# Optimization experiments

Hardware: AMD Instinct MI355X
Metric: run time of the kernel (lower is better)

The kernel has to match this reference:

```python
import jax, jax.numpy as jnp
import numpy as np
import math

B, L, D_MODEL, D_K, H = 2, 1024, 1024, 1024, 16
HD = D_K // H  # 64, even
EPS = 1e-5


def setup_inputs() -> dict:
    key = jax.random.key(0)
    ks = jax.random.split(key, 16)
    s = 0.02
    inp = {
        'word_embed': jax.random.normal(ks[0], (B, L, D_MODEL), jnp.float32),
        'speaker_embed': jax.random.normal(ks[1], (B, L, D_MODEL), jnp.float32),
        'mask': jnp.broadcast_to(jnp.tril(jnp.ones((L, L), jnp.int32)), (B, L, L)),
        'qw_w': jax.random.normal(ks[2], (D_K, D_MODEL), jnp.float32) * s,
        'qw_b': jnp.zeros((D_K,), jnp.float32),
        'kw_w': jax.random.normal(ks[3], (D_K, D_MODEL), jnp.float32) * s,
        'kw_b': jnp.zeros((D_K,), jnp.float32),
        'qs_w': jax.random.normal(ks[4], (D_K, D_MODEL), jnp.float32) * s,
        'qs_b': jnp.zeros((D_K,), jnp.float32),
        'ks_w': jax.random.normal(ks[5], (D_K, D_MODEL), jnp.float32) * s,
        'ks_b': jnp.zeros((D_K,), jnp.float32),
        'v_w': jax.random.normal(ks[6], (D_K, D_MODEL), jnp.float32) * s,
        'v_b': jnp.zeros((D_K,), jnp.float32),
        'out_w': jax.random.normal(ks[7], (D_MODEL, D_K), jnp.float32) * s,
        'out_b': jnp.zeros((D_MODEL,), jnp.float32),
        'gamma': jnp.ones((HD,), jnp.float32),
        'beta': jnp.zeros((HD,), jnp.float32),
    }
    return inp


def _rotary_tables(seq_len, dim, dtype):
    pos = jnp.arange(seq_len, dtype=dtype)[:, None]  # [L,1]
    div = jnp.exp(jnp.arange(0, dim, 2, dtype=dtype) * (-math.log(10000.0) / dim))
    return jnp.sin(pos * div), jnp.cos(pos * div)  # each [L, dim//2]


def _rotary(x, sin, cos):
    # x: [B,H,L,HD]; NOTE: original concatenates halves (non-interleaved output)
    x1, x2 = x[..., 0::2], x[..., 1::2]
    return jnp.concatenate([x1 * cos - x2 * sin, x1 * sin + x2 * cos], axis=-1)


def _layernorm(x, gamma, beta):
    mu = jnp.mean(x, axis=-1, keepdims=True)
    var = jnp.mean(jnp.square(x - mu), axis=-1, keepdims=True)
    return (x - mu) * jax.lax.rsqrt(var + EPS) * gamma + beta


def _split(x):
    b, l, _ = x.shape
    return x.reshape(b, l, H, HD).transpose(0, 2, 1, 3)  # [B,H,L,HD]


def reference(word_embed, speaker_embed, mask, qw_w, qw_b, kw_w, kw_b,
              qs_w, qs_b, ks_w, ks_b, v_w, v_b, out_w, out_b, gamma, beta):
    proj = lambda x, w, b: jnp.einsum('bld,kd->blk', x, w) + b
    qw = _split(proj(word_embed, qw_w, qw_b))
    kw = _split(proj(word_embed, kw_w, kw_b))
    qs = _split(proj(speaker_embed, qs_w, qs_b))
    ks = _split(proj(speaker_embed, ks_w, ks_b))
    v = _split(proj(word_embed, v_w, v_b))

    sin, cos = _rotary_tables(word_embed.shape[1], HD, word_embed.dtype)
    ln = lambda x: _layernorm(_rotary(x, sin, cos), gamma, beta)
    qw, kw, qs, ks = ln(qw), ln(kw), ln(qs), ln(ks)

    scores = (jnp.einsum('bhqd,bhkd->bhqk', qw, kw)
              + jnp.einsum('bhqd,bhkd->bhqk', qs, ks)) / math.sqrt(2 * HD)
    scores = jnp.where(mask[:, None] == 0, -jnp.inf, scores)
    attn = jax.nn.softmax(scores, axis=-1)  # dropout is eval-mode no-op
    out = jnp.einsum('bhqk,bhkd->bhqd', attn, v)
    out = out.transpose(0, 2, 1, 3).reshape(out.shape[0], out.shape[2], D_K)
    out = jnp.einsum('blk,dk->bld', out, out_w) + out_b
    return (out, attn)
```

## Files before the change

### kernel.cpp

```cpp
#include <hip/hip_runtime.h>
#include <cstdint>
#include <cstddef>

typedef __bf16 bf16x8 __attribute__((ext_vector_type(8)));
typedef float  f32x4  __attribute__((ext_vector_type(4)));
typedef unsigned short ushort8_t __attribute__((ext_vector_type(8)));

__device__ __forceinline__ unsigned short f2bf(float f){
  unsigned u = __builtin_bit_cast(unsigned, f);
  u += 0x7fffu + ((u >> 16) & 1u);
  return (unsigned short)(u >> 16);
}
__device__ __forceinline__ float bf2f(unsigned short s){
  return __builtin_bit_cast(float, ((unsigned)s) << 16);
}

#define MFMA16(a,b,c) __builtin_amdgcn_mfma_f32_16x16x32_bf16((a),(b),(c),0,0,0)

__device__ __forceinline__ void gload16(const void* g, void* lds){
  __builtin_amdgcn_global_load_lds(
      (const __attribute__((address_space(1))) void*)g,
      (__attribute__((address_space(3))) void*)lds, 16, 0, 0);
}

#define E_XW    ((size_t)0)
#define E_XS    (E_XW    + (size_t)2048*1024)
#define E_WWORD (E_XS    + (size_t)2048*1024)
#define E_WSPK  (E_WWORD + (size_t)3072*1024)
#define E_WOUT  (E_WSPK  + (size_t)2048*1024)
#define E_PWORD (E_WOUT  + (size_t)1024*1024)
#define E_PSPK  (E_PWORD + (size_t)2048*3072)
#define E_VT    (E_PSPK  + (size_t)2048*2048)
#define E_CTX   (E_VT    + (size_t)2048*1024)
#define E_END   (E_CTX   + (size_t)2048*1024)

__global__ __launch_bounds__(256) void convert_all(
    const float* __restrict__ word, const float* __restrict__ spk,
    const float* __restrict__ qww,  const float* __restrict__ kww,
    const float* __restrict__ vw,   const float* __restrict__ qsw,
    const float* __restrict__ ksw,  const float* __restrict__ outw,
    const float* __restrict__ qwb,  const float* __restrict__ kwb,
    const float* __restrict__ vb,   const float* __restrict__ qsb,
    const float* __restrict__ ksb,
    unsigned short* __restrict__ wsb, float* __restrict__ FB)
{
  int idx = blockIdx.x*256 + threadIdx.x;
  if (idx < 32768){
    int pos = idx >> 5, i = idx & 31;
    float inv = expf((float)(2*i) * -0.14391157f);
    float ang = (float)pos * inv;
    float sv, cv; sincosf(ang, &sv, &cv);
    FB[5120 + idx]         = sv;
    FB[5120 + 32768 + idx] = cv;
  } else if (idx < 33792){
    int i = idx - 32768;
    FB[i] = qwb[i]; FB[1024+i] = kwb[i]; FB[2048+i] = vb[i];
    FB[3072+i] = qsb[i]; FB[3072+1024+i] = ksb[i];
  }

  const size_t total = 2621440;
  for (size_t c = (size_t)blockIdx.x*256 + threadIdx.x; c < total;
       c += (size_t)gridDim.x*256){
    const float* src; size_t dst; size_t i;
    if (c < 524288)       { src = word; dst = E_XW; i = c; }
    else if (c < 1048576) { src = spk;  dst = E_XS; i = c - 524288; }
    else {
      size_t t = c - 1048576; int seg = (int)(t >> 18); i = t & 262143;
      switch (seg){
        case 0:  src = qww; dst = E_WWORD;                      break;
        case 1:  src = kww; dst = E_WWORD + (size_t)1048576;    break;
        case 2:  src = vw;  dst = E_WWORD + (size_t)2097152;    break;
        case 3:  src = qsw; dst = E_WSPK;                       break;
        case 4:  src = ksw; dst = E_WSPK  + (size_t)1048576;    break;
        default: src = outw; dst = E_WOUT;                      break;
      }
    }
    float4 v = ((const float4*)src)[i];
    ushort4 o; o.x = f2bf(v.x); o.y = f2bf(v.y); o.z = f2bf(v.z); o.w = f2bf(v.w);
    ((ushort4*)(wsb + dst))[i] = o;
  }
}

template<int NF>
__device__ __forceinline__ void gemm_body(
    const unsigned short* __restrict__ A, const unsigned short* __restrict__ Bw,
    const float* __restrict__ bias, void* __restrict__ Cv,
    int N, int bid, int out_bf16,
    unsigned short* As, unsigned short* Bs)
{
  const int K = 1024;
  const int BN = NF*32;
  const int nbn = N / BN;
  const int bm = bid / nbn, bn = bid % nbn;
  const int tid = threadIdx.x;
  const int l = tid & 63, w = tid >> 6;
  const int wm = w >> 1, wn = w & 1;
  const int li = l & 15, lg = l >> 4;

  f32x4 acc[4][NF];
  #pragma unroll
  for (int a = 0; a < 4; a++)
    #pragma unroll
    for (int b = 0; b < NF; b++) acc[a][b] = (f32x4){0.f,0.f,0.f,0.f};

  const int colS = (l & 3) * 8;
  const size_t aBase = (size_t)(bm*128) * K;
  const size_t bBase = (size_t)(bn*BN) * K;

  for (int kt = 0; kt < K; kt += 32){
    #pragma unroll
    for (int j = 0; j < 2; j++){
      int row = (w*2 + j)*16 + (l >> 2);
      gload16(A + aBase + (size_t)row*K + kt + colS, &As[(size_t)(w*2+j)*512]);
    }
    if (NF == 4){
      #pragma unroll
      for (int j = 0; j < 2; j++){
        int row = (w*2 + j)*16 + (l >> 2);
        gload16(Bw + bBase + (size_t)row*K + kt + colS, &Bs[(size_t)(w*2+j)*512]);
      }
    } else {
      int row = w*16 + (l >> 2);
      gload16(Bw + bBase + (size_t)row*K + kt + colS, &Bs[(size_t)w*512]);
    }
    asm volatile("s_waitcnt vmcnt(0)" ::: "memory");
    __syncthreads();

    bf16x8 af[4], bfr[NF];
    const int ko = lg * 8;
    #pragma unroll
    for (int fm = 0; fm < 4; fm++)
      af[fm] = *(const bf16x8*)&As[(wm*64 + fm*16 + li)*32 + ko];
    #pragma unroll
    for (int fn = 0; fn < NF; fn++)
      bfr[fn] = *(const bf16x8*)&Bs[(wn*(NF*16) + fn*16 + li)*32 + ko];
    #pragma unroll
    for (int fm = 0; fm < 4; fm++)
      #pragma unroll
      for (int fn = 0; fn < NF; fn++)
        acc[fm][fn] = MFMA16(af[fm], bfr[fn], acc[fm][fn]);
    __syncthreads();
  }

  #pragma unroll
  for (int fm = 0; fm < 4; fm++){
    int m0 = bm*128 + wm*64 + fm*16 + lg*4;
    #pragma unroll
    for (int fn = 0; fn < NF; fn++){
      int n = bn*BN + wn*(NF*16) + fn*16 + li;
      float bv = bias[n];
      #pragma unroll
      for (int r = 0; r < 4; r++){
        float v = acc[fm][fn][r] + bv;
        if (out_bf16) ((unsigned short*)Cv)[(size_t)(m0+r)*N + n] = f2bf(v);
        else          ((float*)Cv)[(size_t)(m0+r)*N + n] = v;
      }
    }
  }
}

__global__ __launch_bounds__(256) void gemm_qkv(
    const unsigned short* __restrict__ XW, const unsigned short* __restrict__ WWORD,
    const unsigned short* __restrict__ XS, const unsigned short* __restrict__ WSPK,
    const float* __restrict__ FB,
    unsigned short* __restrict__ PWORD, unsigned short* __restrict__ PSPK)
{
  __shared__ unsigned short As[128*32];
  __shared__ unsigned short Bs[128*32];
  int raw = blockIdx.x;
  int bid = (raw & 7)*80 + (raw >> 3);
  if (bid < 384)
    gemm_body<4>(XW, WWORD, FB,        PWORD, 3072, bid,       1, As, Bs);
  else
    gemm_body<4>(XS, WSPK,  FB + 3072, PSPK,  2048, bid - 384, 1, As, Bs);
}

__global__ __launch_bounds__(256) void gemm_out(
    const unsigned short* __restrict__ CTX, const unsigned short* __restrict__ WOUT,
    const float* __restrict__ outb, float* __restrict__ outp)
{
  __shared__ unsigned short As[128*32];
  __shared__ unsigned short Bs[64*32];
  int raw = blockIdx.x;
  int bid = (raw & 7)*32 + (raw >> 3);
  gemm_body<2>(CTX, WOUT, outb, outp, 1024, bid, 0, As, Bs);
}

__global__ __launch_bounds__(256) void postproc(
    unsigned short* __restrict__ Pw, unsigned short* __restrict__ Ps,
    const float* __restrict__ gamma, const float* __restrict__ beta,
    const float* __restrict__ TS, const float* __restrict__ TC,
    unsigned short* __restrict__ VT)
{
  __shared__ float lds[2320];
  int bx = blockIdx.x;
  int t = threadIdx.x;
  if (bx < 4096){
    int sec = bx & 3, rp = bx >> 2;
    int half = t >> 7, c = t & 127;
    int row = rp*2 + half;
    int seg = c >> 3, j = c & 7;
    unsigned short* p;
    if      (sec == 0) p = Pw + (size_t)row*3072 +        seg*64;
    else if (sec == 1) p = Pw + (size_t)row*3072 + 1024 + seg*64;
    else if (sec == 2) p = Ps + (size_t)row*2048 +        seg*64;
    else               p = Ps + (size_t)row*2048 + 1024 + seg*64;
    int pos = row & 1023;
    int sl  = half*16 + seg;

    ushort8_t xv = *(const ushort8_t*)(p + j*8);
    float4 sv = *(const float4*)&TS[pos*32 + j*4];
    float4 cv = *(const float4*)&TC[pos*32 + j*4];
    float ss[4] = {sv.x, sv.y, sv.z, sv.w};
    float cc[4] = {cv.x, cv.y, cv.z, cv.w};
    float y1[4], y2[4];
    #pragma unroll
    for (int k = 0; k < 4; k++){
      float x0 = bf2f(xv[2*k]), x1 = bf2f(xv[2*k+1]);
      y1[k] = x0*cc[k] - x1*ss[k];
      y2[k] = x0*ss[k] + x1*cc[k];
    }
    *(float4*)&lds[sl*68 + j*4]      = (float4){y1[0], y1[1], y1[2], y1[3]};
    *(float4*)&lds[sl*68 + 32 + j*4] = (float4){y2[0], y2[1], y2[2], y2[3]};
    __syncthreads();

    float4 a0 = *(const float4*)&lds[sl*68 + j*8];
    float4 a1 = *(const float4*)&lds[sl*68 + j*8 + 4];
    float v[8] = {a0.x, a0.y, a0.z, a0.w, a1.x, a1.y, a1.z, a1.w};
    float s = 0.f;
    #pragma unroll
    for (int k = 0; k < 8; k++) s += v[k];
    #pragma unroll
    for (int o = 1; o < 8; o <<= 1) s += __shfl_xor(s, o);
    float mu = s * (1.f/64.f);
    float sq = 0.f;
    #pragma unroll
    for (int k = 0; k < 8; k++){ float d = v[k] - mu; sq += d*d; }
    #pragma unroll
    for (int o = 1; o < 8; o <<= 1) sq += __shfl_xor(sq, o);
    float rs = rsqrtf(sq * (1.f/64.f) + 1e-5f);
    float4 g0 = *(const float4*)&gamma[j*8], g1 = *(const float4*)&gamma[j*8+4];
    float4 b0 = *(const float4*)&beta[j*8],  b1 = *(const float4*)&beta[j*8+4];
    float gg[8] = {g0.x,g0.y,g0.z,g0.w,g1.x,g1.y,g1.z,g1.w};
    float bb[8] = {b0.x,b0.y,b0.z,b0.w,b1.x,b1.y,b1.z,b1.w};
    ushort8_t o8;
    #pragma unroll
    for (int k = 0; k < 8; k++) o8[k] = f2bf((v[k]-mu)*rs*gg[k] + bb[k]);
    *(ushort8_t*)(p + j*8) = o8;
  } else {
    unsigned short* tp = (unsigned short*)lds;
    int bid2 = bx - 4096;
    int bh = bid2 >> 4, lt = bid2 & 15;
    int b = bh >> 4, h = bh & 15;
    #pragma unroll
    for (int i = 0; i < 2; i++){
      int cc2 = t + i*256;
      int row = cc2 >> 3, co = (cc2 & 7)*8;
      const unsigned short* src = Pw + (size_t)(b*1024 + lt*64 + row)*3072 + 2048 + h*64 + co;
      *(uint4*)&tp[row*72 + co] = *(const uint4*)src;
    }
    __syncthreads();
    int d = t >> 2, jb = (t & 3)*16;
    unsigned short o[16];
    #pragma unroll
    for (int j = 0; j < 16; j++) o[j] = tp[(jb + j)*72 + d];
    unsigned short* dst = VT + ((size_t)bh*64 + d)*1024 + lt*64 + jb;
    *(uint4*)dst       = *(uint4*)&o[0];
    *(uint4*)(dst + 8) = *(uint4*)&o[8];
  }
}

__global__ __launch_bounds__(256) void attn_fused(
    const unsigned short* __restrict__ Pw, const unsigned short* __restrict__ Ps,
    const unsigned short* __restrict__ VTg,
    float* __restrict__ attn, unsigned short* __restrict__ Ctx)
{
  __shared__ unsigned short SL[32256];

  int raw = blockIdx.x;
  int bx  = (raw & 7)*64 + (raw >> 3);
  int b = bx >> 8, rem = bx & 255, h = rem >> 4;
  int qt = 15 - (rem & 15);
  int tid = threadIdx.x;
  int w = tid >> 6, l = tid & 63;
  int lg = l >> 4, li = l & 15;
  int q0 = qt*64 + w*16;
  int bh = b*16 + h;

  int sr = tid >> 3, sc = tid & 7;
  const unsigned short* gKW = Pw + (size_t)(b*1024)*3072 + 1024 + h*64;
  const unsigned short* gKS = Ps + (size_t)(b*1024)*2048 + 1024 + h*64;
  const unsigned short* gVT = VTg + (size_t)bh*64*1024;
  unsigned short* pt = SL + 27648 + w*1152;

  bf16x8 aqw[2], aqs[2];
  {
    int q = q0 + li;
    const unsigned short* pqw = Pw + (size_t)(b*1024 + q)*3072 + h*64 + lg*8;
    const unsigned short* pqs = Ps + (size_t)(b*1024 + q)*2048 + h*64 + lg*8;
    aqw[0] = *(const bf16x8*)pqw;  aqw[1] = *(const bf16x8*)(pqw + 32);
    aqs[0] = *(const bf16x8*)pqs;  aqs[1] = *(const bf16x8*)(pqs + 32);
  }
  const float rscale = 0.08838834764831845f;

  uint4 ka0, ka1, kb0, kb1, va0, va1;

  float ps4[4] = {0.f, 0.f, 0.f, 0.f};
  ka0 = *(const uint4*)(gKW + (size_t)sr*3072 + sc*8);
  ka1 = *(const uint4*)(gKW + (size_t)(sr+32)*3072 + sc*8);
  kb0 = *(const uint4*)(gKS + (size_t)sr*2048 + sc*8);
  kb1 = *(const uint4*)(gKS + (size_t)(sr+32)*2048 + sc*8);
  *(uint4*)(SL + sr*72 + sc*8) = ka0;
  *(uint4*)(SL + (sr+32)*72 + sc*8) = ka1;
  *(uint4*)(SL + 9216 + sr*72 + sc*8) = kb0;
  *(uint4*)(SL + 9216 + (sr+32)*72 + sc*8) = kb1;

  for (int kt = 0; kt <= qt; ++kt){
    int buf = kt & 1;
    if (kt < qt){
      ka0 = *(const uint4*)(gKW + (size_t)((kt+1)*64 + sr)*3072 + sc*8);
      ka1 = *(const uint4*)(gKW + (size_t)((kt+1)*64 + sr+32)*3072 + sc*8);
      kb0 = *(const uint4*)(gKS + (size_t)((kt+1)*64 + sr)*2048 + sc*8);
      kb1 = *(const uint4*)(gKS + (size_t)((kt+1)*64 + sr+32)*2048 + sc*8);
    }
    __syncthreads();
    {
      const unsigned short* KWt = SL + buf*4608;
      const unsigned short* KSt = SL + 9216 + buf*4608;
      f32x4 s[4];
      #pragma unroll
      for (int fn = 0; fn < 4; fn++){
        s[fn] = (f32x4){0.f,0.f,0.f,0.f};
        int rr = (fn*16 + li)*72;
        bf16x8 k0 = *(const bf16x8*)(KWt + rr + lg*8);
        bf16x8 k1 = *(const bf16x8*)(KWt + rr + 32 + lg*8);
        bf16x8 k2 = *(const bf16x8*)(KSt + rr + lg*8);
        bf16x8 k3 = *(const bf16x8*)(KSt + rr + 32 + lg*8);
        s[fn] = MFMA16(aqw[0], k0, s[fn]);
        s[fn] = MFMA16(aqw[1], k1, s[fn]);
        s[fn] = MFMA16(aqs[0], k2, s[fn]);
        s[fn] = MFMA16(aqs[1], k3, s[fn]);
      }
      #pragma unroll
      for (int r = 0; r < 4; r++){
        int q = q0 + lg*4 + r;
        #pragma unroll
        for (int fn = 0; fn < 4; fn++){
          int k = kt*64 + fn*16 + li;
          float e = __expf(s[fn][r] * rscale);
          ps4[r] += (k <= q) ? e : 0.f;
        }
      }
    }
    if (kt < qt){
      int nb = buf ^ 1;
      *(uint4*)(SL + nb*4608 + sr*72 + sc*8) = ka0;
      *(uint4*)(SL + nb*4608 + (sr+32)*72 + sc*8) = ka1;
      *(uint4*)(SL + 9216 + nb*4608 + sr*72 + sc*8) = kb0;
      *(uint4*)(SL + 9216 + nb*4608 + (sr+32)*72 + sc*8) = kb1;
    }
  }
  #pragma unroll
  for (int r = 0; r < 4; r++){
    #pragma unroll
    for (int o = 1; o < 16; o <<= 1) ps4[r] += __shfl_xor(ps4[r], o);
  }
  float rinv[4];
  #pragma unroll
  for (int r = 0; r < 4; r++) rinv[r] = 1.f / ps4[r];

  __syncthreads();
  ka0 = *(const uint4*)(gKW + (size_t)sr*3072 + sc*8);
  ka1 = *(const uint4*)(gKW + (size_t)(sr+32)*3072 + sc*8);
  kb0 = *(const uint4*)(gKS + (size_t)sr*2048 + sc*8);
  kb1 = *(const uint4*)(gKS + (size_t)(sr+32)*2048 + sc*8);
  va0 = *(const uint4*)(gVT + (size_t)sr*1024 + sc*8);
  va1 = *(const uint4*)(gVT + (size_t)(sr+32)*1024 + sc*8);
  *(uint4*)(SL + sr*72 + sc*8) = ka0;
  *(uint4*)(SL + (sr+32)*72 + sc*8) = ka1;
  *(uint4*)(SL + 9216 + sr*72 + sc*8) = kb0;
  *(uint4*)(SL + 9216 + (sr+32)*72 + sc*8) = kb1;
  *(uint4*)(SL + 18432 + sr*72 + sc*8) = va0;
  *(uint4*)(SL + 18432 + (sr+32)*72 + sc*8) = va1;

  f32x4 c[4];
  #pragma unroll
  for (int fn = 0; fn < 4; fn++) c[fn] = (f32x4){0.f,0.f,0.f,0.f};

  for (int kt = 0; kt <= qt; ++kt){
    int buf = kt & 1;
    if (kt < qt){
      ka0 = *(const uint4*)(gKW + (size_t)((kt+1)*64 + sr)*3072 + sc*8);
      ka1 = *(const uint4*)(gKW + (size_t)((kt+1)*64 + sr+32)*3072 + sc*8);
      kb0 = *(const uint4*)(gKS + (size_t)((kt+1)*64 + sr)*2048 + sc*8);
      kb1 = *(const uint4*)(gKS + (size_t)((kt+1)*64 + sr+32)*2048 + sc*8);
      va0 = *(const uint4*)(gVT + (size_t)sr*1024 + (kt+1)*64 + sc*8);
      va1 = *(const uint4*)(gVT + (size_t)(sr+32)*1024 + (kt+1)*64 + sc*8);
    }
    __syncthreads();
    float* abase = attn + ((size_t)bh*1024 + q0 + li)*1024 + kt*64;
    {
      const unsigned short* KWt = SL + buf*4608;
      const unsigned short* KSt = SL + 9216 + buf*4608;
      const unsigned short* VTt = SL + 18432 + buf*4608;
      f32x4 s[4];
      #pragma unroll
      for (int fn = 0; fn < 4; fn++){
        s[fn] = (f32x4){0.f,0.f,0.f,0.f};
        int rr = (fn*16 + li)*72;
        bf16x8 k0 = *(const bf16x8*)(KWt + rr + lg*8);
        bf16x8 k1 = *(const bf16x8*)(KWt + rr + 32 + lg*8);
        bf16x8 k2 = *(const bf16x8*)(KSt + rr + lg*8);
        bf16x8 k3 = *(const bf16x8*)(KSt + rr + 32 + lg*8);
        s[fn] = MFMA16(aqw[0], k0, s[fn]);
        s[fn] = MFMA16(aqw[1], k1, s[fn]);
        s[fn] = MFMA16(aqs[0], k2, s[fn]);
        s[fn] = MFMA16(aqs[1], k3, s[fn]);
      }
      #pragma unroll
      for (int fn = 0; fn < 4; fn++){
        #pragma unroll
        for (int r = 0; r < 4; r++){
          int k = kt*64 + fn*16 + li;
          int q = q0 + lg*4 + r;
          float pp = (k <= q) ? __expf(s[fn][r] * rscale) * rinv[r] : 0.f;
          pt[(lg*4 + r)*72 + fn*16 + li] = f2bf(pp);
        }
      }
      asm volatile("s_waitcnt lgkmcnt(0)" ::: "memory");
      __builtin_amdgcn_sched_barrier(0);
      bf16x8 af0 = *(const bf16x8*)(pt + li*72 + lg*8);
      bf16x8 af1 = *(const bf16x8*)(pt + li*72 + 32 + lg*8);
      ushort8_t u0 = __builtin_bit_cast(ushort8_t, af0);
      ushort8_t u1 = __builtin_bit_cast(ushort8_t, af1);
      *(float4*)(abase + lg*8)          = (float4){bf2f(u0[0]),bf2f(u0[1]),bf2f(u0[2]),bf2f(u0[3])};
      *(float4*)(abase + lg*8 + 4)      = (float4){bf2f(u0[4]),bf2f(u0[5]),bf2f(u0[6]),bf2f(u0[7])};
      *(float4*)(abase + 32 + lg*8)     = (float4){bf2f(u1[0]),bf2f(u1[1]),bf2f(u1[2]),bf2f(u1[3])};
      *(float4*)(abase + 32 + lg*8 + 4) = (float4){bf2f(u1[4]),bf2f(u1[5]),bf2f(u1[6]),bf2f(u1[7])};
      #pragma unroll
      for (int fn = 0; fn < 4; fn++){
        int rr = (fn*16 + li)*72;
        bf16x8 v0 = *(const bf16x8*)(VTt + rr + lg*8);
        bf16x8 v1 = *(const bf16x8*)(VTt + rr + 32 + lg*8);
        c[fn] = MFMA16(af0, v0, c[fn]);
        c[fn] = MFMA16(af1, v1, c[fn]);
      }
    }
    if (kt < qt){
      int nb = buf ^ 1;
      *(uint4*)(SL + nb*4608 + sr*72 + sc*8) = ka0;
      *(uint4*)(SL + nb*4608 + (sr+32)*72 + sc*8) = ka1;
      *(uint4*)(SL + 9216 + nb*4608 + sr*72 + sc*8) = kb0;
      *(uint4*)(SL + 9216 + nb*4608 + (sr+32)*72 + sc*8) = kb1;
      *(uint4*)(SL + 18432 + nb*4608 + sr*72 + sc*8) = va0;
      *(uint4*)(SL + 18432 + nb*4608 + (sr+32)*72 + sc*8) = va1;
    }
  }

  for (int kt = qt + 1; kt < 16; ++kt){
    float* abase = attn + ((size_t)bh*1024 + q0 + li)*1024 + kt*64;
    float4 z = {0.f, 0.f, 0.f, 0.f};
    *(float4*)(abase + lg*8)          = z;
    *(float4*)(abase + lg*8 + 4)      = z;
    *(float4*)(abase + 32 + lg*8)     = z;
    *(float4*)(abase + 32 + lg*8 + 4) = z;
  }

  #pragma unroll
  for (int fn = 0; fn < 4; fn++){
    #pragma unroll
    for (int r = 0; r < 4; r++){
      int q = q0 + lg*4 + r;
      int d = fn*16 + li;
      Ctx[(size_t)(b*1024 + q)*1024 + h*64 + d] = f2bf(c[fn][r]);
    }
  }
}

extern "C" void kernel_launch(void* const* d_in, const int* in_sizes, int n_in,
                              void* d_out, int out_size, void* d_ws, size_t ws_size,
                              hipStream_t stream)
{
  (void)in_sizes; (void)n_in; (void)out_size; (void)ws_size;
  const float* word = (const float*)d_in[0];
  const float* spk  = (const float*)d_in[1];
  const float* qww  = (const float*)d_in[3];
  const float* qwb  = (const float*)d_in[4];
  const float* kww  = (const float*)d_in[5];
  const float* kwb  = (const float*)d_in[6];
  const float* qsw  = (const float*)d_in[7];
  const float* qsb  = (const float*)d_in[8];
  const float* ksw  = (const float*)d_in[9];
  const float* ksb  = (const float*)d_in[10];
  const float* vw   = (const float*)d_in[11];
  const float* vb   = (const float*)d_in[12];
  const float* outw = (const float*)d_in[13];
  const float* outb = (const float*)d_in[14];
  const float* gamma= (const float*)d_in[15];
  const float* beta = (const float*)d_in[16];

  unsigned short* U = (unsigned short*)d_ws;
  unsigned short* XW    = U + E_XW;
  unsigned short* XS    = U + E_XS;
  unsigned short* WWORD = U + E_WWORD;
  unsigned short* WSPK  = U + E_WSPK;
  unsigned short* WOUT  = U + E_WOUT;
  unsigned short* PWORD = U + E_PWORD;
  unsigned short* PSPK  = U + E_PSPK;
  unsigned short* VT    = U + E_VT;
  unsigned short* CTX   = U + E_CTX;
  float* FB = (float*)(U + E_END);
  float* TS = FB + 5120;
  float* TC = TS + 32768;

  float* outp = (float*)d_out;
  float* attn = outp + (size_t)2*1024*1024;

  convert_all<<<4096, 256, 0, stream>>>(word, spk, qww, kww, vw, qsw, ksw, outw,
                                        qwb, kwb, vb, qsb, ksb, U, FB);
  gemm_qkv<<<640, 256, 0, stream>>>(XW, WWORD, XS, WSPK, FB, PWORD, PSPK);
  postproc<<<4608, 256, 0, stream>>>(PWORD, PSPK, gamma, beta, TS, TC, VT);
  attn_fused<<<512, 256, 0, stream>>>(PWORD, PSPK, VT, attn, CTX);
  gemm_out<<<256, 256, 0, stream>>>(CTX, WOUT, outb, outp);
}
```

Baseline: 121.1 us.

## Split attention key tiles across two wave halves with 512-thread blocks

Doubles the attn_fused block to 512 threads. Each group of four waves takes half of each 64-key tile, for both the row-sum pass and the PV pass. Partial softmax denominators and partial context accumulators are combined through shared memory, and each thread now does one global-to-LDS load per tensor instead of two. The aim is more waves per block to hide latency and less per-wave serial work, at the cost of extra barriers, an LDS reduction and higher per-block resource use.

```diff
diff --git a/kernel.cpp b/kernel.cpp
--- a/kernel.cpp
+++ b/kernel.cpp
@@ -270,12 +270,12 @@
   }
 }
 
-__global__ __launch_bounds__(256) void attn_fused(
+__global__ __launch_bounds__(512) void attn_fused(
     const unsigned short* __restrict__ Pw, const unsigned short* __restrict__ Ps,
     const unsigned short* __restrict__ VTg,
     float* __restrict__ attn, unsigned short* __restrict__ Ctx)
 {
-  __shared__ unsigned short SL[32256];
+  __shared__ unsigned short SL[36864];
 
   int raw = blockIdx.x;
   int bx  = (raw & 7)*64 + (raw >> 3);
@@ -283,8 +283,9 @@
   int qt = 15 - (rem & 15);
   int tid = threadIdx.x;
   int w = tid >> 6, l = tid & 63;
+  int ws = w & 3, hf = w >> 2;
   int lg = l >> 4, li = l & 15;
-  int q0 = qt*64 + w*16;
+  int q0 = qt*64 + ws*16;
   int bh = b*16 + h;
 
   int sr = tid >> 3, sc = tid & 7;
@@ -292,6 +293,8 @@
   const unsigned short* gKS = Ps + (size_t)(b*1024)*2048 + 1024 + h*64;
   const unsigned short* gVT = VTg + (size_t)bh*64*1024;
   unsigned short* pt = SL + 27648 + w*1152;
+  float* SLf = (float*)(SL + 27648);
+  float* SLc = (float*)SL;
 
   bf16x8 aqw[2], aqs[2];
   {
@@ -303,61 +306,54 @@
   }
   const float rscale = 0.08838834764831845f;
 
-  uint4 ka0, ka1, kb0, kb1, va0, va1;
+  uint4 ka, kb, va;
 
   float ps4[4] = {0.f, 0.f, 0.f, 0.f};
-  ka0 = *(const uint4*)(gKW + (size_t)sr*3072 + sc*8);
-  ka1 = *(const uint4*)(gKW + (size_t)(sr+32)*3072 + sc*8);
-  kb0 = *(const uint4*)(gKS + (size_t)sr*2048 + sc*8);
-  kb1 = *(const uint4*)(gKS + (size_t)(sr+32)*2048 + sc*8);
-  *(uint4*)(SL + sr*72 + sc*8) = ka0;
-  *(uint4*)(SL + (sr+32)*72 + sc*8) = ka1;
-  *(uint4*)(SL + 9216 + sr*72 + sc*8) = kb0;
-  *(uint4*)(SL + 9216 + (sr+32)*72 + sc*8) = kb1;
+  ka = *(const uint4*)(gKW + (size_t)sr*3072 + sc*8);
+  kb = *(const uint4*)(gKS + (size_t)sr*2048 + sc*8);
+  *(uint4*)(SL + sr*72 + sc*8) = ka;
+  *(uint4*)(SL + 9216 + sr*72 + sc*8) = kb;
 
   for (int kt = 0; kt <= qt; ++kt){
     int buf = kt & 1;
     if (kt < qt){
-      ka0 = *(const uint4*)(gKW + (size_t)((kt+1)*64 + sr)*3072 + sc*8);
-      ka1 = *(const uint4*)(gKW + (size_t)((kt+1)*64 + sr+32)*3072 + sc*8);
-      kb0 = *(const uint4*)(gKS + (size_t)((kt+1)*64 + sr)*2048 + sc*8);
-      kb1 = *(const uint4*)(gKS + (size_t)((kt+1)*64 + sr+32)*2048 + sc*8);
+      ka = *(const uint4*)(gKW + (size_t)((kt+1)*64 + sr)*3072 + sc*8);
+      kb = *(const uint4*)(gKS + (size_t)((kt+1)*64 + sr)*2048 + sc*8);
     }
     __syncthreads();
     {
       const unsigned short* KWt = SL + buf*4608;
       const unsigned short* KSt = SL + 9216 + buf*4608;
-      f32x4 s[4];
-      #pragma unroll
-      for (int fn = 0; fn < 4; fn++){
-        s[fn] = (f32x4){0.f,0.f,0.f,0.f};
+      f32x4 s[2];
+      #pragma unroll
+      for (int f = 0; f < 2; f++){
+        int fn = hf*2 + f;
+        s[f] = (f32x4){0.f,0.f,0.f,0.f};
         int rr = (fn*16 + li)*72;
         bf16x8 k0 = *(const bf16x8*)(KWt + rr + lg*8);
         bf16x8 k1 = *(const bf16x8*)(KWt + rr + 32 + lg*8);
         bf16x8 k2 = *(const bf16x8*)(KSt + rr + lg*8);
         bf16x8 k3 = *(const bf16x8*)(KSt + rr + 32 + lg*8);
-        s[fn] = MFMA16(aqw[0], k0, s[fn]);
-        s[fn] = MFMA16(aqw[1], k1, s[fn]);
-        s[fn] = MFMA16(aqs[0], k2, s[fn]);
-        s[fn] = MFMA16(aqs[1], k3, s[fn]);
+        s[f] = MFMA16(aqw[0], k0, s[f]);
+        s[f] = MFMA16(aqw[1], k1, s[f]);
+        s[f] = MFMA16(aqs[0], k2, s[f]);
+        s[f] = MFMA16(aqs[1], k3, s[f]);
       }
       #pragma unroll
       for (int r = 0; r < 4; r++){
         int q = q0 + lg*4 + r;
         #pragma unroll
-        for (int fn = 0; fn < 4; fn++){
-          int k = kt*64 + fn*16 + li;
-          float e = __expf(s[fn][r] * rscale);
+        for (int f = 0; f < 2; f++){
+          int k = kt*64 + (hf*2 + f)*16 + li;
+          float e = __expf(s[f][r] * rscale);
           ps4[r] += (k <= q) ? e : 0.f;
         }
       }
     }
     if (kt < qt){
       int nb = buf ^ 1;
-      *(uint4*)(SL + nb*4608 + sr*72 + sc*8) = ka0;
-      *(uint4*)(SL + nb*4608 + (sr+32)*72 + sc*8) = ka1;
-      *(uint4*)(SL + 9216 + nb*4608 + sr*72 + sc*8) = kb0;
-      *(uint4*)(SL + 9216 + nb*4608 + (sr+32)*72 + sc*8) = kb1;
+      *(uint4*)(SL + nb*4608 + sr*72 + sc*8) = ka;
+      *(uint4*)(SL + 9216 + nb*4608 + sr*72 + sc*8) = kb;
     }
   }
   #pragma unroll
@@ -365,23 +361,24 @@
     #pragma unroll
     for (int o = 1; o < 16; o <<= 1) ps4[r] += __shfl_xor(ps4[r], o);
   }
+  __syncthreads();
+  if (li == 0){
+    #pragma unroll
+    for (int r = 0; r < 4; r++) SLf[w*16 + lg*4 + r] = ps4[r];
+  }
+  __syncthreads();
   float rinv[4];
   #pragma unroll
-  for (int r = 0; r < 4; r++) rinv[r] = 1.f / ps4[r];
+  for (int r = 0; r < 4; r++)
+    rinv[r] = 1.f / (ps4[r] + SLf[(w ^ 4)*16 + lg*4 + r]);
 
   __syncthreads();
-  ka0 = *(const uint4*)(gKW + (size_t)sr*3072 + sc*8);
-  ka1 = *(const uint4*)(gKW + (size_t)(sr+32)*3072 + sc*8);
-  kb0 = *(const uint4*)(gKS + (size_t)sr*2048 + sc*8);
-  kb1 = *(const uint4*)(gKS + (size_t)(sr+32)*2048 + sc*8);
-  va0 = *(const uint4*)(gVT + (size_t)sr*1024 + sc*8);
-  va1 = *(const uint4*)(gVT + (size_t)(sr+32)*1024 + sc*8);
-  *(uint4*)(SL + sr*72 + sc*8) = ka0;
-  *(uint4*)(SL + (sr+32)*72 + sc*8) = ka1;
-  *(uint4*)(SL + 9216 + sr*72 + sc*8) = kb0;
-  *(uint4*)(SL + 9216 + (sr+32)*72 + sc*8) = kb1;
-  *(uint4*)(SL + 18432 + sr*72 + sc*8) = va0;
-  *(uint4*)(SL + 18432 + (sr+32)*72 + sc*8) = va1;
+  ka = *(const uint4*)(gKW + (size_t)sr*3072 + sc*8);
+  kb = *(const uint4*)(gKS + (size_t)sr*2048 + sc*8);
+  va = *(const uint4*)(gVT + (size_t)sr*1024 + sc*8);
+  *(uint4*)(SL + sr*72 + sc*8) = ka;
+  *(uint4*)(SL + 9216 + sr*72 + sc*8) = kb;
+  *(uint4*)(SL + 18432 + sr*72 + sc*8) = va;
 
   f32x4 c[4];
   #pragma unroll
@@ -390,89 +387,91 @@
   for (int kt = 0; kt <= qt; ++kt){
     int buf = kt & 1;
     if (kt < qt){
-      ka0 = *(const uint4*)(gKW + (size_t)((kt+1)*64 + sr)*3072 + sc*8);
-      ka1 = *(const uint4*)(gKW + (size_t)((kt+1)*64 + sr+32)*3072 + sc*8);
-      kb0 = *(const uint4*)(gKS + (size_t)((kt+1)*64 + sr)*2048 + sc*8);
-      kb1 = *(const uint4*)(gKS + (size_t)((kt+1)*64 + sr+32)*2048 + sc*8);
-      va0 = *(const uint4*)(gVT + (size_t)sr*1024 + (kt+1)*64 + sc*8);
-      va1 = *(const uint4*)(gVT + (size_t)(sr+32)*1024 + (kt+1)*64 + sc*8);
+      ka = *(const uint4*)(gKW + (size_t)((kt+1)*64 + sr)*3072 + sc*8);
+      kb = *(const uint4*)(gKS + (size_t)((kt+1)*64 + sr)*2048 + sc*8);
+      va = *(const uint4*)(gVT + (size_t)sr*1024 + (kt+1)*64 + sc*8);
     }
     __syncthreads();
-    float* abase = attn + ((size_t)bh*1024 + q0 + li)*1024 + kt*64;
     {
       const unsigned short* KWt = SL + buf*4608;
       const unsigned short* KSt = SL + 9216 + buf*4608;
       const unsigned short* VTt = SL + 18432 + buf*4608;
-      f32x4 s[4];
-      #pragma unroll
-      for (int fn = 0; fn < 4; fn++){
-        s[fn] = (f32x4){0.f,0.f,0.f,0.f};
+      f32x4 s[2];
+      #pragma unroll
+      for (int f = 0; f < 2; f++){
+        int fn = hf*2 + f;
+        s[f] = (f32x4){0.f,0.f,0.f,0.f};
         int rr = (fn*16 + li)*72;
         bf16x8 k0 = *(const bf16x8*)(KWt + rr + lg*8);
         bf16x8 k1 = *(const bf16x8*)(KWt + rr + 32 + lg*8);
         bf16x8 k2 = *(const bf16x8*)(KSt + rr + lg*8);
         bf16x8 k3 = *(const bf16x8*)(KSt + rr + 32 + lg*8);
-        s[fn] = MFMA16(aqw[0], k0, s[fn]);
-        s[fn] = MFMA16(aqw[1], k1, s[fn]);
-        s[fn] = MFMA16(aqs[0], k2, s[fn]);
-        s[fn] = MFMA16(aqs[1], k3, s[fn]);
-      }
-      #pragma unroll
-      for (int fn = 0; fn < 4; fn++){
+        s[f] = MFMA16(aqw[0], k0, s[f]);
+        s[f] = MFMA16(aqw[1], k1, s[f]);
+        s[f] = MFMA16(aqs[0], k2, s[f]);
+        s[f] = MFMA16(aqs[1], k3, s[f]);
+      }
+      #pragma unroll
+      for (int f = 0; f < 2; f++){
+        int fn = hf*2 + f;
         #pragma unroll
         for (int r = 0; r < 4; r++){
           int k = kt*64 + fn*16 + li;
           int q = q0 + lg*4 + r;
-          float pp = (k <= q) ? __expf(s[fn][r] * rscale) * rinv[r] : 0.f;
+          float pp = (k <= q) ? __expf(s[f][r] * rscale) * rinv[r] : 0.f;
           pt[(lg*4 + r)*72 + fn*16 + li] = f2bf(pp);
         }
       }
       asm volatile("s_waitcnt lgkmcnt(0)" ::: "memory");
       __builtin_amdgcn_sched_barrier(0);
-      bf16x8 af0 = *(const bf16x8*)(pt + li*72 + lg*8);
-      bf16x8 af1 = *(const bf16x8*)(pt + li*72 + 32 + lg*8);
-      ushort8_t u0 = __builtin_bit_cast(ushort8_t, af0);
-      ushort8_t u1 = __builtin_bit_cast(ushort8_t, af1);
-      *(float4*)(abase + lg*8)          = (float4){bf2f(u0[0]),bf2f(u0[1]),bf2f(u0[2]),bf2f(u0[3])};
-      *(float4*)(abase + lg*8 + 4)      = (float4){bf2f(u0[4]),bf2f(u0[5]),bf2f(u0[6]),bf2f(u0[7])};
-      *(float4*)(abase + 32 + lg*8)     = (float4){bf2f(u1[0]),bf2f(u1[1]),bf2f(u1[2]),bf2f(u1[3])};
-      *(float4*)(abase + 32 + lg*8 + 4) = (float4){bf2f(u1[4]),bf2f(u1[5]),bf2f(u1[6]),bf2f(u1[7])};
-      #pragma unroll
-      for (int fn = 0; fn < 4; fn++){
-        int rr = (fn*16 + li)*72;
-        bf16x8 v0 = *(const bf16x8*)(VTt + rr + lg*8);
-        bf16x8 v1 = *(const bf16x8*)(VTt + rr + 32 + lg*8);
-        c[fn] = MFMA16(af0, v0, c[fn]);
-        c[fn] = MFMA16(af1, v1, c[fn]);
+      bf16x8 af = *(const bf16x8*)(pt + li*72 + hf*32 + lg*8);
+      ushort8_t u = __builtin_bit_cast(ushort8_t, af);
+      float* abase = attn + ((size_t)bh*1024 + q0 + li)*1024 + kt*64 + hf*32;
+      *(float4*)(abase + lg*8)     = (float4){bf2f(u[0]),bf2f(u[1]),bf2f(u[2]),bf2f(u[3])};
+      *(float4*)(abase + lg*8 + 4) = (float4){bf2f(u[4]),bf2f(u[5]),bf2f(u[6]),bf2f(u[7])};
+      #pragma unroll
+      for (int fn2 = 0; fn2 < 4; fn2++){
+        int rr = (fn2*16 + li)*72;
+        bf16x8 v = *(const bf16x8*)(VTt + rr + hf*32 + lg*8);
+        c[fn2] = MFMA16(af, v, c[fn2]);
       }
     }
     if (kt < qt){
       int nb = buf ^ 1;
-      *(uint4*)(SL + nb*4608 + sr*72 + sc*8) = ka0;
-      *(uint4*)(SL + nb*4608 + (sr+32)*72 + sc*8) = ka1;
-      *(uint4*)(SL + 9216 + nb*4608 + sr*72 + sc*8) = kb0;
-      *(uint4*)(SL + 9216 + nb*4608 + (sr+32)*72 + sc*8) = kb1;
-      *(uint4*)(SL + 18432 + nb*4608 + sr*72 + sc*8) = va0;
-      *(uint4*)(SL + 18432 + nb*4608 + (sr+32)*72 + sc*8) = va1;
+      *(uint4*)(SL + nb*4608 + sr*72 + sc*8) = ka;
+      *(uint4*)(SL + 9216 + nb*4608 + sr*72 + sc*8) = kb;
+      *(uint4*)(SL + 18432 + nb*4608 + sr*72 + sc*8) = va;
     }
   }
 
   for (int kt = qt + 1; kt < 16; ++kt){
-    float* abase = attn + ((size_t)bh*1024 + q0 + li)*1024 + kt*64;
+    float* abase = attn + ((size_t)bh*1024 + q0 + li)*1024 + kt*64 + hf*32;
     float4 z = {0.f, 0.f, 0.f, 0.f};
-    *(float4*)(abase + lg*8)          = z;
-    *(float4*)(abase + lg*8 + 4)      = z;
-    *(float4*)(abase + 32 + lg*8)     = z;
-    *(float4*)(abase + 32 + lg*8 + 4) = z;
-  }
-
-  #pragma unroll
-  for (int fn = 0; fn < 4; fn++){
-    #pragma unroll
-    for (int r = 0; r < 4; r++){
-      int q = q0 + lg*4 + r;
-      int d = fn*16 + li;
-      Ctx[(size_t)(b*1024 + q)*1024 + h*64 + d] = f2bf(c[fn][r]);
+    *(float4*)(abase + lg*8)     = z;
+    *(float4*)(abase + lg*8 + 4) = z;
+  }
+
+  __syncthreads();
+  if (hf == 1){
+    #pragma unroll
+    for (int fn2 = 0; fn2 < 4; fn2++)
+      *(f32x4*)&SLc[(ws*64 + l)*20 + fn2*4] = c[fn2];
+  }
+  __syncthreads();
+  if (hf == 0){
+    #pragma unroll
+    for (int fn2 = 0; fn2 < 4; fn2++){
+      f32x4 cp = *(const f32x4*)&SLc[(ws*64 + l)*20 + fn2*4];
+      c[fn2] += cp;
+    }
+    #pragma unroll
+    for (int fn2 = 0; fn2 < 4; fn2++){
+      #pragma unroll
+      for (int r = 0; r < 4; r++){
+        int q = q0 + lg*4 + r;
+        int d = fn2*16 + li;
+        Ctx[(size_t)(b*1024 + q)*1024 + h*64 + d] = f2bf(c[fn2][r]);
+      }
     }
   }
 }
@@ -520,6 +519,6 @@
                                         qwb, kwb, vb, qsb, ksb, U, FB);
   gemm_qkv<<<640, 256, 0, stream>>>(XW, WWORD, XS, WSPK, FB, PWORD, PSPK);
   postproc<<<4608, 256, 0, stream>>>(PWORD, PSPK, gamma, beta, TS, TC, VT);
-  attn_fused<<<512, 256, 0, stream>>>(PWORD, PSPK, VT, attn, CTX);
+  attn_fused<<<512, 512, 0, stream>>>(PWORD, PSPK, VT, attn, CTX);
   gemm_out<<<256, 256, 0, stream>>>(CTX, WOUT, outb, outp);
 }
```

New measurement: 117.5 us, median of 2. 1.03x faster.
